# Optimization experiments

Hardware: AMD Instinct MI355X
Metric: run time of the kernel (lower is better)

The kernel has to match this reference:

```python
import jax, jax.numpy as jnp
import numpy as np

B, DIM, H, W = 64, 512, 16, 20
HID = DIM // 2          # 256, MutualAttention hidden
HEADS = 8
NZ, NX = 64, 256        # template (8x8) and search (16x16) token counts
EPS_NORM = 1e-12
EPS_LN = 1e-5


def setup_inputs() -> dict:
    key = jax.random.key(0)
    ks = jax.random.split(key, 16)
    s = 0.02
    return {
        "x1": jax.random.normal(ks[0], (B, DIM, H, W), jnp.float32),
        "x2": jax.random.normal(ks[1], (B, DIM, H, W), jnp.float32),
        "W_lin": jax.random.normal(ks[2], (DIM, 2 * DIM), jnp.float32) * s,
        "b_lin": jnp.zeros((2 * DIM,), jnp.float32),
        "W_down": jax.random.normal(ks[3], (DIM, HID), jnp.float32) * s,
        "b_down": jnp.zeros((HID,), jnp.float32),
        "W_up": jax.random.normal(ks[4], (HID, DIM), jnp.float32) * s,
        "b_up": jnp.zeros((DIM,), jnp.float32),
        "Wq": jax.random.normal(ks[5], (HID, HID), jnp.float32) * s,
        "Wk": jax.random.normal(ks[6], (HID, HID), jnp.float32) * s,
        "Wv": jax.random.normal(ks[7], (HID, HID), jnp.float32) * s,
        "Wo": jax.random.normal(ks[8], (HID, HID), jnp.float32) * s,
        "temperature": jnp.ones((HEADS, 1, 1), jnp.float32),
        "W_end": jax.random.normal(ks[9], (DIM, DIM), jnp.float32) * s,
        "b_end": jnp.zeros((DIM,), jnp.float32),
        "gamma": jnp.ones((DIM,), jnp.float32),
        "beta": jnp.zeros((DIM,), jnp.float32),
    }


def _l2norm(x):
    n = jnp.sqrt(jnp.sum(x * x, axis=-1, keepdims=True))
    return x / jnp.maximum(n, EPS_NORM)


def _branch(zx, zy, W_down, b_down, W_up, b_up, Wq, Wk, Wv, Wo, temperature):
    # zx, zy: [B, n, DIM] tokens; conv1x1 == per-token linear so spatial reshape is a no-op
    res = zx
    a = jax.nn.relu(zx @ W_down + b_down)   # [B, n, HID]  (k, v source)
    b_ = jax.nn.relu(zy @ W_down + b_down)  # [B, n, HID]  (q source)
    xb = jnp.swapaxes(a, 1, 2)              # [B, HID, n]
    yb = jnp.swapaxes(b_, 1, 2)
    res1 = xb
    q = jnp.einsum('oc,bcn->bon', Wq, yb)
    k = jnp.einsum('oc,bcn->bon', Wk, xb)
    v = jnp.einsum('oc,bcn->bon', Wv, xb)
    bsz, _, n = q.shape
    c = HID // HEADS
    q = _l2norm(q.reshape(bsz, HEADS, c, n))
    k = _l2norm(k.reshape(bsz, HEADS, c, n))
    v = v.reshape(bsz, HEADS, c, n)
    attn = jnp.einsum('bhcn,bhdn->bhcd', q, k) * temperature  # [B, H, c, c]
    attn = jax.nn.softmax(attn, axis=-1)
    out = jnp.einsum('bhcd,bhdn->bhcn', attn, v).reshape(bsz, HID, n)
    out = jnp.einsum('oc,bcn->bon', Wo, out)
    out = res1 + out                          # [B, HID, n]
    tok = jnp.swapaxes(out, 1, 2)             # [B, n, HID]
    return res + tok @ W_up + b_up            # [B, n, DIM]


def reference(x1, x2, W_lin, b_lin, W_down, b_down, W_up, b_up,
              Wq, Wk, Wv, Wo, temperature, W_end, b_end, gamma, beta):
    bsz = x1.shape[0]
    t1 = jnp.swapaxes(x1.reshape(bsz, DIM, H * W), 1, 2)  # [B, N, DIM]
    t2 = jnp.swapaxes(x2.reshape(bsz, DIM, H * W), 1, 2)
    h1 = jax.nn.relu(t1 @ W_lin + b_lin)
    h2 = jax.nn.relu(t2 @ W_lin + b_lin)
    y1, u1 = h1[..., :DIM], h1[..., DIM:]
    y2, u2 = h2[..., :DIM], h2[..., DIM:]
    # MutualAttention: template tokens (first 64) and search tokens (rest)
    o_z = _branch(u1[:, :NZ], u2[:, :NZ], W_down, b_down, W_up, b_up, Wq, Wk, Wv, Wo, temperature)
    o_x = _branch(u1[:, NZ:], u2[:, NZ:], W_down, b_down, W_up, b_up, Wq, Wk, Wv, Wo, temperature)
    v1 = jnp.concatenate([o_z, o_x], axis=1)  # [B, N, DIM]
    y = y1 + v1
    pre = t1 + (y @ W_end + b_end)
    mu = jnp.mean(pre, axis=-1, keepdims=True)
    var = jnp.mean((pre - mu) ** 2, axis=-1, keepdims=True)
    ln = (pre - mu) / jnp.sqrt(var + EPS_LN) * gamma + beta
    return jnp.swapaxes(ln, 1, 2).reshape(bsz, DIM, H, W)
```

## Files before the change

kernel.cpp:

```cpp
#include <hip/hip_runtime.h>
#include <math.h>

#define NTOK 320
#define BB   64
#define DIMC 512
#define HIDC 256
#define NHEAD 8

#define F_BIAS 1
#define F_RELU 2
#define F_RES1 4
#define F_RES2 8

#define BM 128
#define BN 64
#define BK 32

typedef __attribute__((ext_vector_type(8))) short bf8_t;
typedef __attribute__((ext_vector_type(4))) float f4_t;

__device__ __forceinline__ void bsplit(float f, short& h, short& l) {
    const unsigned u = __float_as_uint(f);
    h = (short)(u >> 16);
    const float fh = __uint_as_float(u & 0xffff0000u);
    const float fl = f - fh;
    l = (short)(__float_as_uint(fl) >> 16);
}

template<int FLAGS>
__global__ __launch_bounds__(256)
void gemm_mfma(const float* __restrict__ W, int ldw,
               const float* __restrict__ X, long sX,
               float* __restrict__ C, long sC,
               int Dk,
               const float* __restrict__ bias,
               const float* __restrict__ R1, long sR1,
               const float* __restrict__ R2, long sR2)
{
    __shared__ float Ws[BK][BM];
    __shared__ float Xs[BK][BN];

    const int b  = blockIdx.z;
    const int j0 = blockIdx.x * BM;
    const int n0 = blockIdx.y * BN;
    const float* Xb = X + (long)b * sX;

    const int t    = threadIdx.x;
    const int wave = t >> 6;
    const int lane = t & 63;
    const int wm   = wave >> 1;
    const int wn   = wave & 1;
    const int r16  = lane & 15;
    const int g    = lane >> 4;

    f4_t acc[4][2];
    #pragma unroll
    for (int i = 0; i < 4; ++i)
        #pragma unroll
        for (int j = 0; j < 2; ++j)
            acc[i][j] = (f4_t){0.f, 0.f, 0.f, 0.f};

    for (int d0 = 0; d0 < Dk; d0 += BK) {
        #pragma unroll
        for (int i = 0; i < 4; ++i) {
            const int slot = t + (i << 8);
            const int k = slot >> 5;
            const int c = slot & 31;
            const f4_t v = *(const f4_t*)&W[(long)(d0 + k) * ldw + j0 + (c << 2)];
            const int cs = c ^ ((k >> 3) << 2);
            *(f4_t*)&Ws[k][cs << 2] = v;
        }
        #pragma unroll
        for (int i = 0; i < 2; ++i) {
            const int slot = t + (i << 8);
            const int k = slot >> 4;
            const int c = slot & 15;
            const f4_t v = *(const f4_t*)&Xb[(long)(d0 + k) * NTOK + n0 + (c << 2)];
            const int cs = c ^ ((k >> 3) << 2);
            *(f4_t*)&Xs[k][cs << 2] = v;
        }
        __syncthreads();

        bf8_t ah[4], al[4], bh[2], bl[2];
        #pragma unroll
        for (int fm = 0; fm < 4; ++fm) {
            const int m  = wm * 64 + fm * 16 + r16;
            const int col = (((m >> 2) ^ (g << 2)) << 2) | (m & 3);
            #pragma unroll
            for (int e = 0; e < 8; ++e) {
                short h, l;
                bsplit(Ws[g * 8 + e][col], h, l);
                ah[fm][e] = h; al[fm][e] = l;
            }
        }
        #pragma unroll
        for (int fn = 0; fn < 2; ++fn) {
            const int n  = wn * 32 + fn * 16 + r16;
            const int col = (((n >> 2) ^ (g << 2)) << 2) | (n & 3);
            #pragma unroll
            for (int e = 0; e < 8; ++e) {
                short h, l;
                bsplit(Xs[g * 8 + e][col], h, l);
                bh[fn][e] = h; bl[fn][e] = l;
            }
        }

        #pragma unroll
        for (int fm = 0; fm < 4; ++fm)
            #pragma unroll
            for (int fn = 0; fn < 2; ++fn) {
                acc[fm][fn] = __builtin_amdgcn_mfma_f32_16x16x32_bf16(ah[fm], bh[fn], acc[fm][fn], 0, 0, 0);
                acc[fm][fn] = __builtin_amdgcn_mfma_f32_16x16x32_bf16(ah[fm], bl[fn], acc[fm][fn], 0, 0, 0);
                acc[fm][fn] = __builtin_amdgcn_mfma_f32_16x16x32_bf16(al[fm], bh[fn], acc[fm][fn], 0, 0, 0);
            }
        __syncthreads();
    }

    float* Cb = C + (long)b * sC;
    #pragma unroll
    for (int fm = 0; fm < 4; ++fm) {
        #pragma unroll
        for (int reg = 0; reg < 4; ++reg) {
            const int m = j0 + wm * 64 + fm * 16 + g * 4 + reg;
            float bv = 0.f;
            if (FLAGS & F_BIAS) bv = bias[m];
            #pragma unroll
            for (int fn = 0; fn < 2; ++fn) {
                const int n = n0 + wn * 32 + fn * 16 + r16;
                float v = acc[fm][fn][reg] + bv;
                if (FLAGS & F_RES1) v += R1[(long)b * sR1 + (long)m * NTOK + n];
                if (FLAGS & F_RES2) v += R2[(long)b * sR2 + (long)m * NTOK + n];
                if (FLAGS & F_RELU) v = fmaxf(v, 0.f);
                Cb[(long)m * NTOK + n] = v;
            }
        }
    }
}

__global__ __launch_bounds__(256)
void transpose4_k(const float* __restrict__ Wq, const float* __restrict__ Wk,
                  const float* __restrict__ Wv, const float* __restrict__ Wo,
                  float* __restrict__ out)
{
    __shared__ float tile[32][33];
    const float* src = (blockIdx.z == 0) ? Wq : (blockIdx.z == 1) ? Wk
                     : (blockIdx.z == 2) ? Wv : Wo;
    float* dst = out + (long)blockIdx.z * 65536;
    const int x0 = blockIdx.x << 5, y0 = blockIdx.y << 5;
    const int tx = threadIdx.x & 31, ty = threadIdx.x >> 5;
    for (int i = ty; i < 32; i += 8)
        tile[i][tx] = src[(long)(y0 + i) * 256 + x0 + tx];
    __syncthreads();
    for (int i = ty; i < 32; i += 8)
        dst[(long)(x0 + i) * 256 + y0 + tx] = tile[tx][i];
}

__global__ __launch_bounds__(256)
void attn_kernel(const float* __restrict__ Q, const float* __restrict__ K,
                 const float* __restrict__ V, float* __restrict__ O,
                 const float* __restrict__ temp)
{
    const int slice = blockIdx.x;
    const int h     = blockIdx.y;
    const int b     = blockIdx.z;
    const int n0    = slice ? 64 : 0;
    const int Nt    = slice ? 256 : 64;

    __shared__ float qs[32][260], ks[32][260], vs[32][260];
    __shared__ float P[32][36];
    __shared__ float invq[32], invk[32];

    const long base = (long)b * HIDC * NTOK + (long)h * 32 * NTOK + n0;
    const int t = threadIdx.x;
    const int nf4 = Nt >> 2;

    for (int idx = t; idx < 32 * nf4; idx += 256) {
        const int r  = idx / nf4;
        const int n4 = (idx % nf4) << 2;
        *(float4*)&qs[r][n4] = *(const float4*)&Q[base + (long)r * NTOK + n4];
        *(float4*)&ks[r][n4] = *(const float4*)&K[base + (long)r * NTOK + n4];
        *(float4*)&vs[r][n4] = *(const float4*)&V[base + (long)r * NTOK + n4];
    }
    __syncthreads();

    {
        const int r = t >> 3, l8 = t & 7;
        float sq = 0.f, sk = 0.f;
        for (int k4 = l8; k4 < nf4; k4 += 8) {
            const float4 a = *(const float4*)&qs[r][k4 << 2];
            sq = fmaf(a.x,a.x, fmaf(a.y,a.y, fmaf(a.z,a.z, fmaf(a.w,a.w, sq))));
            const float4 c = *(const float4*)&ks[r][k4 << 2];
            sk = fmaf(c.x,c.x, fmaf(c.y,c.y, fmaf(c.z,c.z, fmaf(c.w,c.w, sk))));
        }
        sq += __shfl_xor(sq, 1); sq += __shfl_xor(sq, 2); sq += __shfl_xor(sq, 4);
        sk += __shfl_xor(sk, 1); sk += __shfl_xor(sk, 2); sk += __shfl_xor(sk, 4);
        if (l8 == 0) {
            invq[r] = 1.f / fmaxf(sqrtf(sq), 1e-12f);
            invk[r] = 1.f / fmaxf(sqrtf(sk), 1e-12f);
        }
    }
    __syncthreads();

    {
        const int c = t >> 3, db = (t & 7) << 2;
        float s0 = 0.f, s1 = 0.f, s2 = 0.f, s3 = 0.f;
        for (int n = 0; n < Nt; n += 4) {
            const float4 qv = *(const float4*)&qs[c][n];
            const float4 k0 = *(const float4*)&ks[db + 0][n];
            const float4 k1 = *(const float4*)&ks[db + 1][n];
            const float4 k2 = *(const float4*)&ks[db + 2][n];
            const float4 k3 = *(const float4*)&ks[db + 3][n];
            s0 = fmaf(qv.x,k0.x, fmaf(qv.y,k0.y, fmaf(qv.z,k0.z, fmaf(qv.w,k0.w, s0))));
            s1 = fmaf(qv.x,k1.x, fmaf(qv.y,k1.y, fmaf(qv.z,k1.z, fmaf(qv.w,k1.w, s1))));
            s2 = fmaf(qv.x,k2.x, fmaf(qv.y,k2.y, fmaf(qv.z,k2.z, fmaf(qv.w,k2.w, s2))));
            s3 = fmaf(qv.x,k3.x, fmaf(qv.y,k3.y, fmaf(qv.z,k3.z, fmaf(qv.w,k3.w, s3))));
        }
        const float sc = invq[c] * temp[h];
        float l0 = s0 * sc * invk[db + 0];
        float l1 = s1 * sc * invk[db + 1];
        float l2 = s2 * sc * invk[db + 2];
        float l3 = s3 * sc * invk[db + 3];
        float m = fmaxf(fmaxf(l0, l1), fmaxf(l2, l3));
        m = fmaxf(m, __shfl_xor(m, 1));
        m = fmaxf(m, __shfl_xor(m, 2));
        m = fmaxf(m, __shfl_xor(m, 4));
        const float e0 = expf(l0 - m), e1 = expf(l1 - m);
        const float e2 = expf(l2 - m), e3 = expf(l3 - m);
        float sum = e0 + e1 + e2 + e3;
        sum += __shfl_xor(sum, 1); sum += __shfl_xor(sum, 2); sum += __shfl_xor(sum, 4);
        const float inv = 1.f / sum;
        P[c][db + 0] = e0 * inv; P[c][db + 1] = e1 * inv;
        P[c][db + 2] = e2 * inv; P[c][db + 3] = e3 * inv;
    }
    __syncthreads();

    for (int idx = t; idx < 32 * nf4; idx += 256) {
        const int c  = idx / nf4;
        const int n4 = (idx % nf4) << 2;
        float4 o = make_float4(0.f, 0.f, 0.f, 0.f);
        #pragma unroll
        for (int d = 0; d < 32; ++d) {
            const float p = P[c][d];
            const float4 vv = *(const float4*)&vs[d][n4];
            o.x = fmaf(p, vv.x, o.x); o.y = fmaf(p, vv.y, o.y);
            o.z = fmaf(p, vv.z, o.z); o.w = fmaf(p, vv.w, o.w);
        }
        *(float4*)&O[base + (long)c * NTOK + n4] = o;
    }
}

__global__ __launch_bounds__(256)
void ln_kernel(const float* __restrict__ Pre, const float* __restrict__ gamma,
               const float* __restrict__ beta, float* __restrict__ out)
{
    const int b  = blockIdx.y;
    const int n  = (blockIdx.x << 6) + (threadIdx.x & 63);
    const int q  = threadIdx.x >> 6;
    const float* Pb = Pre + (long)b * DIMC * NTOK;
    float s = 0.f, s2 = 0.f;
    for (int d = q; d < DIMC; d += 4) {
        const float v = Pb[(long)d * NTOK + n];
        s += v; s2 = fmaf(v, v, s2);
    }
    __shared__ float sb[4][64], s2b[4][64];
    sb[q][threadIdx.x & 63] = s;
    s2b[q][threadIdx.x & 63] = s2;
    __syncthreads();
    float ts = 0.f, ts2 = 0.f;
    #pragma unroll
    for (int i = 0; i < 4; ++i) { ts += sb[i][threadIdx.x & 63]; ts2 += s2b[i][threadIdx.x & 63]; }
    const float mu   = ts * (1.f / 512.f);
    const float var  = ts2 * (1.f / 512.f) - mu * mu;
    const float rstd = 1.f / sqrtf(var + 1e-5f);
    float* Ob = out + (long)b * DIMC * NTOK;
    for (int d = q; d < DIMC; d += 4) {
        const float v = Pb[(long)d * NTOK + n];
        Ob[(long)d * NTOK + n] = (v - mu) * rstd * gamma[d] + beta[d];
    }
}

extern "C" void kernel_launch(void* const* d_in, const int* in_sizes, int n_in,
                              void* d_out, int out_size, void* d_ws, size_t ws_size,
                              hipStream_t stream)
{
    const float* x1     = (const float*)d_in[0];
    const float* x2     = (const float*)d_in[1];
    const float* W_lin  = (const float*)d_in[2];
    const float* b_lin  = (const float*)d_in[3];
    const float* W_down = (const float*)d_in[4];
    const float* b_down = (const float*)d_in[5];
    const float* W_up   = (const float*)d_in[6];
    const float* b_up   = (const float*)d_in[7];
    const float* Wq     = (const float*)d_in[8];
    const float* Wk     = (const float*)d_in[9];
    const float* Wv     = (const float*)d_in[10];
    const float* Wo     = (const float*)d_in[11];
    const float* temp   = (const float*)d_in[12];
    const float* W_end  = (const float*)d_in[13];
    const float* b_end  = (const float*)d_in[14];
    const float* gamma  = (const float*)d_in[15];
    const float* beta   = (const float*)d_in[16];

    float* ws = (float*)d_ws;
    const long s512  = (long)DIMC * NTOK;
    const long s1024 = 2L * s512;
    const long s256  = (long)HIDC * NTOK;

    float* H1  = ws;
    float* U2  = H1 + (long)BB * 1024 * NTOK;
    float* XB  = U2 + (long)BB * 512 * NTOK;
    float* YB  = XB + (long)BB * 256 * NTOK;
    float* Qb  = YB + (long)BB * 256 * NTOK;
    float* Kb  = Qb + (long)BB * 256 * NTOK;
    float* Vb  = Kb + (long)BB * 256 * NTOK;
    float* WT  = Vb + (long)BB * 256 * NTOK;
    float* Y1   = H1;
    float* U1   = H1 + 512 * NTOK;
    float* AO   = YB;
    float* OUTC = Qb;
    float* PRE  = U2;

    const dim3 blk(256);

    transpose4_k<<<dim3(8, 8, 4), blk, 0, stream>>>(Wq, Wk, Wv, Wo, WT);

    gemm_mfma<F_BIAS | F_RELU><<<dim3(8, 5, BB), blk, 0, stream>>>(
        W_lin, 1024, x1, s512, H1, s1024, 512, b_lin, nullptr, 0, nullptr, 0);
    gemm_mfma<F_BIAS | F_RELU><<<dim3(4, 5, BB), blk, 0, stream>>>(
        W_lin + 512, 1024, x2, s512, U2, s512, 512, b_lin + 512, nullptr, 0, nullptr, 0);
    gemm_mfma<F_BIAS | F_RELU><<<dim3(2, 5, BB), blk, 0, stream>>>(
        W_down, 256, U1, s1024, XB, s256, 512, b_down, nullptr, 0, nullptr, 0);
    gemm_mfma<F_BIAS | F_RELU><<<dim3(2, 5, BB), blk, 0, stream>>>(
        W_down, 256, U2, s512, YB, s256, 512, b_down, nullptr, 0, nullptr, 0);
    gemm_mfma<0><<<dim3(2, 5, BB), blk, 0, stream>>>(
        WT + 0 * 65536, 256, YB, s256, Qb, s256, 256, nullptr, nullptr, 0, nullptr, 0);
    gemm_mfma<0><<<dim3(2, 5, BB), blk, 0, stream>>>(
        WT + 1 * 65536, 256, XB, s256, Kb, s256, 256, nullptr, nullptr, 0, nullptr, 0);
    gemm_mfma<0><<<dim3(2, 5, BB), blk, 0, stream>>>(
        WT + 2 * 65536, 256, XB, s256, Vb, s256, 256, nullptr, nullptr, 0, nullptr, 0);
    attn_kernel<<<dim3(2, NHEAD, BB), blk, 0, stream>>>(Qb, Kb, Vb, AO, temp);
    gemm_mfma<F_RES1><<<dim3(2, 5, BB), blk, 0, stream>>>(
        WT + 3 * 65536, 256, AO, s256, OUTC, s256, 256, nullptr, XB, s256, nullptr, 0);
    gemm_mfma<F_BIAS | F_RES1 | F_RES2><<<dim3(4, 5, BB), blk, 0, stream>>>(
        W_up, 512, OUTC, s256, Y1, s1024, 256, b_up, U1, s1024, Y1, s1024);
    gemm_mfma<F_BIAS | F_RES1><<<dim3(4, 5, BB), blk, 0, stream>>>(
        W_end, 512, Y1, s1024, PRE, s512, 512, b_end, x1, s512, nullptr, 0);
    ln_kernel<<<dim3(5, BB), blk, 0, stream>>>(PRE, gamma, beta, (float*)d_out);
}
```

Before: 648.7 us.

## Switch pipeline to token-major layout with pre-split bf16 hi/lo operands

Reworks the whole pipeline to a token-major row layout. Inputs and weights are pre-split once into bf16 high/low halves, so the GEMM inner loop loads ready MFMA fragments from LDS instead of splitting floats on every tile. Intermediates are stored as packed bf16 pairs, K and V are fused into one GEMM, and the attention and layernorm kernels are rewritten for the new layout. This adds extra packing kernels and transposes and doubles the number of intermediate buffers written, in exchange for less per-tile conversion work and contiguous fragment loads.

```diff
diff --git a/kernel.cpp b/kernel.cpp
--- a/kernel.cpp
+++ b/kernel.cpp
@@ -3,55 +3,105 @@
 
 #define NTOK 320
 #define BB   64
+#define RTOT (BB * NTOK)
 #define DIMC 512
 #define HIDC 256
 #define NHEAD 8
 
-#define F_BIAS 1
-#define F_RELU 2
-#define F_RES1 4
-#define F_RES2 8
-
-#define BM 128
-#define BN 64
-#define BK 32
-
+typedef unsigned short u16;
 typedef __attribute__((ext_vector_type(8))) short bf8_t;
 typedef __attribute__((ext_vector_type(4))) float f4_t;
-
-__device__ __forceinline__ void bsplit(float f, short& h, short& l) {
+typedef __attribute__((ext_vector_type(4))) unsigned short us4_t;
+typedef __attribute__((ext_vector_type(4))) unsigned int  u4_t;
+
+#define F_BIAS  1
+#define F_RELU  2
+#define F_F32   4
+#define F_PACK  8
+#define F_RES1P 16
+#define F_RES2P 32
+#define F_RESX1 64
+
+__device__ __forceinline__ void bsplit(float f, u16& h, u16& l) {
     const unsigned u = __float_as_uint(f);
-    h = (short)(u >> 16);
-    const float fh = __uint_as_float(u & 0xffff0000u);
-    const float fl = f - fh;
-    l = (short)(__float_as_uint(fl) >> 16);
+    h = (u16)(u >> 16);
+    const float fl = f - __uint_as_float(u & 0xffff0000u);
+    l = (u16)(__float_as_uint(fl) >> 16);
+}
+__device__ __forceinline__ float brecon(u16 h, u16 l) {
+    return __uint_as_float((unsigned)h << 16) + __uint_as_float((unsigned)l << 16);
+}
+
+__global__ __launch_bounds__(256)
+void pack_w_k(const float* __restrict__ Wlin, const float* __restrict__ Wdown,
+              const float* __restrict__ Wup,  const float* __restrict__ Wend,
+              const float* __restrict__ Wq,   const float* __restrict__ Wk,
+              const float* __restrict__ Wv,   const float* __restrict__ Wo,
+              u16* __restrict__ Ph, u16* __restrict__ Pl)
+{
+    const int idx = blockIdx.x * 256 + threadIdx.x;
+    if (idx >= 1310720) return;
+    float v;
+    int i = idx;
+    if      (i < 524288) { const int j = i >> 9, d = i & 511; v = Wlin[d * 1024 + j]; }
+    else if (i < 655360) { i -= 524288; const int j = i >> 9, d = i & 511; v = Wdown[d * 256 + j]; }
+    else if (i < 786432) { i -= 655360; const int j = i >> 8, d = i & 255; v = Wup[d * 512 + j]; }
+    else if (i < 1048576){ i -= 786432; const int j = i >> 9, d = i & 511; v = Wend[d * 512 + j]; }
+    else if (i < 1114112){ v = Wq[i - 1048576]; }
+    else if (i < 1245184){ i -= 1114112; v = (i < 65536) ? Wk[i] : Wv[i - 65536]; }
+    else                 { v = Wo[i - 1245184]; }
+    u16 h, l; bsplit(v, h, l);
+    Ph[idx] = h; Pl[idx] = l;
+}
+
+__global__ __launch_bounds__(256)
+void pack_x_k(const float* __restrict__ x1, const float* __restrict__ x2,
+              u16* __restrict__ X1h, u16* __restrict__ X1l,
+              u16* __restrict__ X2h, u16* __restrict__ X2l)
+{
+    __shared__ float tile[64 * 65];
+    const int b = blockIdx.z & 63, which = blockIdx.z >> 6;
+    const float* src = which ? x2 : x1;
+    u16* Dh = which ? X2h : X1h;
+    u16* Dl = which ? X2l : X1l;
+    const int c0 = blockIdx.x << 6, n0 = blockIdx.y << 6;
+    const int t = threadIdx.x, col = t & 63, rq = t >> 6;
+    const float* sb_ = src + (long)b * DIMC * NTOK;
+    #pragma unroll
+    for (int i = 0; i < 16; ++i) {
+        const int c = rq * 16 + i;
+        tile[c * 65 + col] = sb_[(long)(c0 + c) * NTOK + n0 + col];
+    }
+    __syncthreads();
+    #pragma unroll
+    for (int i = 0; i < 16; ++i) {
+        const int nr = rq * 16 + i;
+        u16 h, l; bsplit(tile[col * 65 + nr], h, l);
+        const long o = (long)(b * NTOK + n0 + nr) * DIMC + c0 + col;
+        Dh[o] = h; Dl[o] = l;
+    }
 }
 
 template<int FLAGS>
 __global__ __launch_bounds__(256)
-void gemm_mfma(const float* __restrict__ W, int ldw,
-               const float* __restrict__ X, long sX,
-               float* __restrict__ C, long sC,
-               int Dk,
-               const float* __restrict__ bias,
-               const float* __restrict__ R1, long sR1,
-               const float* __restrict__ R2, long sR2)
-{
-    __shared__ float Ws[BK][BM];
-    __shared__ float Xs[BK][BN];
-
-    const int b  = blockIdx.z;
-    const int j0 = blockIdx.x * BM;
-    const int n0 = blockIdx.y * BN;
-    const float* Xb = X + (long)b * sX;
-
-    const int t    = threadIdx.x;
-    const int wave = t >> 6;
-    const int lane = t & 63;
-    const int wm   = wave >> 1;
-    const int wn   = wave & 1;
-    const int r16  = lane & 15;
-    const int g    = lane >> 4;
+void gemm_tm(const u16* __restrict__ Agh, const u16* __restrict__ Agl,
+             const u16* __restrict__ Bgh, const u16* __restrict__ Bgl,
+             int Dk,
+             float* __restrict__ Cf, int ldcf,
+             u16* __restrict__ Ch, u16* __restrict__ Cl, int ldcp,
+             const float* __restrict__ bias,
+             const u16* __restrict__ R1h, const u16* __restrict__ R1l, int ldr1,
+             const u16* __restrict__ R2h, const u16* __restrict__ R2l, int ldr2,
+             const float* __restrict__ xres)
+{
+    __shared__ __align__(16) u16 Ah[128 * 40], Al[128 * 40];
+    __shared__ __align__(16) u16 Bh[64 * 40],  Bl[64 * 40];
+
+    const int j0 = blockIdx.x * 128;
+    const int r0 = blockIdx.y * 64;
+    const int t = threadIdx.x, lane = t & 63, wave = t >> 6;
+    const int wm = wave >> 1, wn = wave & 1;
+    const int r16 = lane & 15, g = lane >> 4;
 
     f4_t acc[4][2];
     #pragma unroll
@@ -60,51 +110,35 @@
         for (int j = 0; j < 2; ++j)
             acc[i][j] = (f4_t){0.f, 0.f, 0.f, 0.f};
 
-    for (int d0 = 0; d0 < Dk; d0 += BK) {
-        #pragma unroll
-        for (int i = 0; i < 4; ++i) {
-            const int slot = t + (i << 8);
-            const int k = slot >> 5;
-            const int c = slot & 31;
-            const f4_t v = *(const f4_t*)&W[(long)(d0 + k) * ldw + j0 + (c << 2)];
-            const int cs = c ^ ((k >> 3) << 2);
-            *(f4_t*)&Ws[k][cs << 2] = v;
-        }
-        #pragma unroll
-        for (int i = 0; i < 2; ++i) {
-            const int slot = t + (i << 8);
-            const int k = slot >> 4;
-            const int c = slot & 15;
-            const f4_t v = *(const f4_t*)&Xb[(long)(d0 + k) * NTOK + n0 + (c << 2)];
-            const int cs = c ^ ((k >> 3) << 2);
-            *(f4_t*)&Xs[k][cs << 2] = v;
+    for (int d0 = 0; d0 < Dk; d0 += 32) {
+        {
+            const int row0 = t >> 2,        c0_ = (t & 3) << 3;
+            const int row1 = (t >> 2) + 64;
+            const long a0 = (long)(j0 + row0) * Dk + d0 + c0_;
+            const long a1 = (long)(j0 + row1) * Dk + d0 + c0_;
+            *(u4_t*)&Ah[row0 * 40 + c0_] = *(const u4_t*)&Agh[a0];
+            *(u4_t*)&Ah[row1 * 40 + c0_] = *(const u4_t*)&Agh[a1];
+            *(u4_t*)&Al[row0 * 40 + c0_] = *(const u4_t*)&Agl[a0];
+            *(u4_t*)&Al[row1 * 40 + c0_] = *(const u4_t*)&Agl[a1];
+            const long ab = (long)(r0 + row0) * Dk + d0 + c0_;
+            *(u4_t*)&Bh[row0 * 40 + c0_] = *(const u4_t*)&Bgh[ab];
+            *(u4_t*)&Bl[row0 * 40 + c0_] = *(const u4_t*)&Bgl[ab];
         }
         __syncthreads();
 
         bf8_t ah[4], al[4], bh[2], bl[2];
         #pragma unroll
         for (int fm = 0; fm < 4; ++fm) {
-            const int m  = wm * 64 + fm * 16 + r16;
-            const int col = (((m >> 2) ^ (g << 2)) << 2) | (m & 3);
-            #pragma unroll
-            for (int e = 0; e < 8; ++e) {
-                short h, l;
-                bsplit(Ws[g * 8 + e][col], h, l);
-                ah[fm][e] = h; al[fm][e] = l;
-            }
+            const int m = wm * 64 + fm * 16 + r16;
+            ah[fm] = *(const bf8_t*)&Ah[m * 40 + g * 8];
+            al[fm] = *(const bf8_t*)&Al[m * 40 + g * 8];
         }
         #pragma unroll
         for (int fn = 0; fn < 2; ++fn) {
-            const int n  = wn * 32 + fn * 16 + r16;
-            const int col = (((n >> 2) ^ (g << 2)) << 2) | (n & 3);
-            #pragma unroll
-            for (int e = 0; e < 8; ++e) {
-                short h, l;
-                bsplit(Xs[g * 8 + e][col], h, l);
-                bh[fn][e] = h; bl[fn][e] = l;
-            }
-        }
-
+            const int rr = wn * 32 + fn * 16 + r16;
+            bh[fn] = *(const bf8_t*)&Bh[rr * 40 + g * 8];
+            bl[fn] = *(const bf8_t*)&Bl[rr * 40 + g * 8];
+        }
         #pragma unroll
         for (int fm = 0; fm < 4; ++fm)
             #pragma unroll
@@ -116,87 +150,88 @@
         __syncthreads();
     }
 
-    float* Cb = C + (long)b * sC;
+    const int bb = r0 / NTOK, nn0 = r0 % NTOK;
     #pragma unroll
     for (int fm = 0; fm < 4; ++fm) {
-        #pragma unroll
-        for (int reg = 0; reg < 4; ++reg) {
-            const int m = j0 + wm * 64 + fm * 16 + g * 4 + reg;
-            float bv = 0.f;
-            if (FLAGS & F_BIAS) bv = bias[m];
-            #pragma unroll
-            for (int fn = 0; fn < 2; ++fn) {
-                const int n = n0 + wn * 32 + fn * 16 + r16;
-                float v = acc[fm][fn][reg] + bv;
-                if (FLAGS & F_RES1) v += R1[(long)b * sR1 + (long)m * NTOK + n];
-                if (FLAGS & F_RES2) v += R2[(long)b * sR2 + (long)m * NTOK + n];
-                if (FLAGS & F_RELU) v = fmaxf(v, 0.f);
-                Cb[(long)m * NTOK + n] = v;
+        const int jb = j0 + wm * 64 + fm * 16 + g * 4;
+        f4_t bv = (f4_t){0.f, 0.f, 0.f, 0.f};
+        if (FLAGS & F_BIAS) bv = *(const f4_t*)&bias[jb];
+        #pragma unroll
+        for (int fn = 0; fn < 2; ++fn) {
+            const int r = r0 + wn * 32 + fn * 16 + r16;
+            f4_t v = acc[fm][fn];
+            if (FLAGS & F_BIAS) v += bv;
+            if (FLAGS & F_RES1P) {
+                const us4_t rh = *(const us4_t*)&R1h[(long)r * ldr1 + jb];
+                const us4_t rl = *(const us4_t*)&R1l[(long)r * ldr1 + jb];
+                #pragma unroll
+                for (int q = 0; q < 4; ++q) v[q] += brecon(rh[q], rl[q]);
+            }
+            if (FLAGS & F_RES2P) {
+                const us4_t rh = *(const us4_t*)&R2h[(long)r * ldr2 + jb];
+                const us4_t rl = *(const us4_t*)&R2l[(long)r * ldr2 + jb];
+                #pragma unroll
+                for (int q = 0; q < 4; ++q) v[q] += brecon(rh[q], rl[q]);
+            }
+            if (FLAGS & F_RESX1) {
+                const int nl = nn0 + wn * 32 + fn * 16 + r16;
+                #pragma unroll
+                for (int q = 0; q < 4; ++q)
+                    v[q] += xres[(long)bb * DIMC * NTOK + (long)(jb + q) * NTOK + nl];
+            }
+            if (FLAGS & F_RELU) {
+                #pragma unroll
+                for (int q = 0; q < 4; ++q) v[q] = fmaxf(v[q], 0.f);
+            }
+            if (FLAGS & F_F32)
+                *(f4_t*)&Cf[(long)r * ldcf + jb] = v;
+            if (FLAGS & F_PACK) {
+                us4_t h4, l4;
+                #pragma unroll
+                for (int q = 0; q < 4; ++q) { u16 h, l; bsplit(v[q], h, l); h4[q] = h; l4[q] = l; }
+                *(us4_t*)&Ch[(long)r * ldcp + jb] = h4;
+                *(us4_t*)&Cl[(long)r * ldcp + jb] = l4;
             }
         }
     }
 }
 
 __global__ __launch_bounds__(256)
-void transpose4_k(const float* __restrict__ Wq, const float* __restrict__ Wk,
-                  const float* __restrict__ Wv, const float* __restrict__ Wo,
-                  float* __restrict__ out)
-{
-    __shared__ float tile[32][33];
-    const float* src = (blockIdx.z == 0) ? Wq : (blockIdx.z == 1) ? Wk
-                     : (blockIdx.z == 2) ? Wv : Wo;
-    float* dst = out + (long)blockIdx.z * 65536;
-    const int x0 = blockIdx.x << 5, y0 = blockIdx.y << 5;
-    const int tx = threadIdx.x & 31, ty = threadIdx.x >> 5;
-    for (int i = ty; i < 32; i += 8)
-        tile[i][tx] = src[(long)(y0 + i) * 256 + x0 + tx];
-    __syncthreads();
-    for (int i = ty; i < 32; i += 8)
-        dst[(long)(x0 + i) * 256 + y0 + tx] = tile[tx][i];
-}
-
-__global__ __launch_bounds__(256)
-void attn_kernel(const float* __restrict__ Q, const float* __restrict__ K,
-                 const float* __restrict__ V, float* __restrict__ O,
-                 const float* __restrict__ temp)
-{
-    const int slice = blockIdx.x;
-    const int h     = blockIdx.y;
-    const int b     = blockIdx.z;
-    const int n0    = slice ? 64 : 0;
-    const int Nt    = slice ? 256 : 64;
-
-    __shared__ float qs[32][260], ks[32][260], vs[32][260];
-    __shared__ float P[32][36];
+void attn_tm(const float* __restrict__ Qf, const float* __restrict__ KVf,
+             u16* __restrict__ AOh, u16* __restrict__ AOl,
+             const float* __restrict__ temp)
+{
+    const int slice = blockIdx.x, h = blockIdx.y, b = blockIdx.z;
+    const int rb = b * NTOK + (slice ? 64 : 0);
+    const int Nt = slice ? 256 : 64;
+    const int qc = h * 32;
+
+    __shared__ float ks[256 * 33], vs[256 * 33];
+    __shared__ float PT[32 * 36];
     __shared__ float invq[32], invk[32];
-
-    const long base = (long)b * HIDC * NTOK + (long)h * 32 * NTOK + n0;
     const int t = threadIdx.x;
-    const int nf4 = Nt >> 2;
-
-    for (int idx = t; idx < 32 * nf4; idx += 256) {
-        const int r  = idx / nf4;
-        const int n4 = (idx % nf4) << 2;
-        *(float4*)&qs[r][n4] = *(const float4*)&Q[base + (long)r * NTOK + n4];
-        *(float4*)&ks[r][n4] = *(const float4*)&K[base + (long)r * NTOK + n4];
-        *(float4*)&vs[r][n4] = *(const float4*)&V[base + (long)r * NTOK + n4];
+
+    for (int q = t; q < Nt * 8; q += 256) {
+        const int n = q >> 3, c4 = (q & 7) << 2;
+        *(f4_t*)&ks[n * 33 + c4] = *(const f4_t*)&KVf[(long)(rb + n) * 512 + qc + c4];
+        *(f4_t*)&vs[n * 33 + c4] = *(const f4_t*)&KVf[(long)(rb + n) * 512 + 256 + qc + c4];
     }
     __syncthreads();
 
     {
-        const int r = t >> 3, l8 = t & 7;
+        const int c = t >> 3, l8 = t & 7;
         float sq = 0.f, sk = 0.f;
-        for (int k4 = l8; k4 < nf4; k4 += 8) {
-            const float4 a = *(const float4*)&qs[r][k4 << 2];
-            sq = fmaf(a.x,a.x, fmaf(a.y,a.y, fmaf(a.z,a.z, fmaf(a.w,a.w, sq))));
-            const float4 c = *(const float4*)&ks[r][k4 << 2];
-            sk = fmaf(c.x,c.x, fmaf(c.y,c.y, fmaf(c.z,c.z, fmaf(c.w,c.w, sk))));
+        for (int n = l8; n < Nt; n += 8) {
+            const float qv = Qf[(long)(rb + n) * 256 + qc + c];
+            sq = fmaf(qv, qv, sq);
+            const float kv = ks[n * 33 + c];
+            sk = fmaf(kv, kv, sk);
         }
         sq += __shfl_xor(sq, 1); sq += __shfl_xor(sq, 2); sq += __shfl_xor(sq, 4);
         sk += __shfl_xor(sk, 1); sk += __shfl_xor(sk, 2); sk += __shfl_xor(sk, 4);
         if (l8 == 0) {
-            invq[r] = 1.f / fmaxf(sqrtf(sq), 1e-12f);
-            invk[r] = 1.f / fmaxf(sqrtf(sk), 1e-12f);
+            invq[c] = 1.f / fmaxf(sqrtf(sq), 1e-12f);
+            invk[c] = 1.f / fmaxf(sqrtf(sk), 1e-12f);
         }
     }
     __syncthreads();
@@ -205,77 +240,104 @@
         const int c = t >> 3, db = (t & 7) << 2;
         float s0 = 0.f, s1 = 0.f, s2 = 0.f, s3 = 0.f;
         for (int n = 0; n < Nt; n += 4) {
-            const float4 qv = *(const float4*)&qs[c][n];
-            const float4 k0 = *(const float4*)&ks[db + 0][n];
-            const float4 k1 = *(const float4*)&ks[db + 1][n];
-            const float4 k2 = *(const float4*)&ks[db + 2][n];
-            const float4 k3 = *(const float4*)&ks[db + 3][n];
-            s0 = fmaf(qv.x,k0.x, fmaf(qv.y,k0.y, fmaf(qv.z,k0.z, fmaf(qv.w,k0.w, s0))));
-            s1 = fmaf(qv.x,k1.x, fmaf(qv.y,k1.y, fmaf(qv.z,k1.z, fmaf(qv.w,k1.w, s1))));
-            s2 = fmaf(qv.x,k2.x, fmaf(qv.y,k2.y, fmaf(qv.z,k2.z, fmaf(qv.w,k2.w, s2))));
-            s3 = fmaf(qv.x,k3.x, fmaf(qv.y,k3.y, fmaf(qv.z,k3.z, fmaf(qv.w,k3.w, s3))));
+            #pragma unroll
+            for (int u = 0; u < 4; ++u) {
+                const float qv = Qf[(long)(rb + n + u) * 256 + qc + c];
+                const int o = (n + u) * 33 + db;
+                s0 = fmaf(qv, ks[o + 0], s0);
+                s1 = fmaf(qv, ks[o + 1], s1);
+                s2 = fmaf(qv, ks[o + 2], s2);
+                s3 = fmaf(qv, ks[o + 3], s3);
+            }
         }
         const float sc = invq[c] * temp[h];
-        float l0 = s0 * sc * invk[db + 0];
-        float l1 = s1 * sc * invk[db + 1];
-        float l2 = s2 * sc * invk[db + 2];
-        float l3 = s3 * sc * invk[db + 3];
+        const float l0 = s0 * sc * invk[db + 0];
+        const float l1 = s1 * sc * invk[db + 1];
+        const float l2 = s2 * sc * invk[db + 2];
+        const float l3 = s3 * sc * invk[db + 3];
         float m = fmaxf(fmaxf(l0, l1), fmaxf(l2, l3));
         m = fmaxf(m, __shfl_xor(m, 1));
         m = fmaxf(m, __shfl_xor(m, 2));
         m = fmaxf(m, __shfl_xor(m, 4));
         const float e0 = expf(l0 - m), e1 = expf(l1 - m);
         const float e2 = expf(l2 - m), e3 = expf(l3 - m);
-        float sum = e0 + e1 + e2 + e3;
-        sum += __shfl_xor(sum, 1); sum += __shfl_xor(sum, 2); sum += __shfl_xor(sum, 4);
-        const float inv = 1.f / sum;
-        P[c][db + 0] = e0 * inv; P[c][db + 1] = e1 * inv;
-        P[c][db + 2] = e2 * inv; P[c][db + 3] = e3 * inv;
-    }
-    __syncthreads();
-
-    for (int idx = t; idx < 32 * nf4; idx += 256) {
-        const int c  = idx / nf4;
-        const int n4 = (idx % nf4) << 2;
-        float4 o = make_float4(0.f, 0.f, 0.f, 0.f);
-        #pragma unroll
+        float s = e0 + e1 + e2 + e3;
+        s += __shfl_xor(s, 1); s += __shfl_xor(s, 2); s += __shfl_xor(s, 4);
+        const float inv = 1.f / s;
+        PT[(db + 0) * 36 + c] = e0 * inv;
+        PT[(db + 1) * 36 + c] = e1 * inv;
+        PT[(db + 2) * 36 + c] = e2 * inv;
+        PT[(db + 3) * 36 + c] = e3 * inv;
+    }
+    __syncthreads();
+
+    for (int idx = t; idx < Nt * 8; idx += 256) {
+        const int n = idx >> 3, cq = (idx & 7) << 2;
+        f4_t o = (f4_t){0.f, 0.f, 0.f, 0.f};
+        #pragma unroll 8
         for (int d = 0; d < 32; ++d) {
-            const float p = P[c][d];
-            const float4 vv = *(const float4*)&vs[d][n4];
-            o.x = fmaf(p, vv.x, o.x); o.y = fmaf(p, vv.y, o.y);
-            o.z = fmaf(p, vv.z, o.z); o.w = fmaf(p, vv.w, o.w);
-        }
-        *(float4*)&O[base + (long)c * NTOK + n4] = o;
+            const float vv = vs[n * 33 + d];
+            const f4_t p = *(const f4_t*)&PT[d * 36 + cq];
+            o += p * vv;
+        }
+        us4_t h4, l4;
+        #pragma unroll
+        for (int q = 0; q < 4; ++q) { u16 h, l; bsplit(o[q], h, l); h4[q] = h; l4[q] = l; }
+        const long oadr = (long)(rb + n) * 256 + qc + cq;
+        *(us4_t*)&AOh[oadr] = h4;
+        *(us4_t*)&AOl[oadr] = l4;
     }
 }
 
 __global__ __launch_bounds__(256)
-void ln_kernel(const float* __restrict__ Pre, const float* __restrict__ gamma,
-               const float* __restrict__ beta, float* __restrict__ out)
-{
-    const int b  = blockIdx.y;
-    const int n  = (blockIdx.x << 6) + (threadIdx.x & 63);
-    const int q  = threadIdx.x >> 6;
-    const float* Pb = Pre + (long)b * DIMC * NTOK;
-    float s = 0.f, s2 = 0.f;
-    for (int d = q; d < DIMC; d += 4) {
-        const float v = Pb[(long)d * NTOK + n];
-        s += v; s2 = fmaf(v, v, s2);
-    }
-    __shared__ float sb[4][64], s2b[4][64];
-    sb[q][threadIdx.x & 63] = s;
-    s2b[q][threadIdx.x & 63] = s2;
-    __syncthreads();
-    float ts = 0.f, ts2 = 0.f;
-    #pragma unroll
-    for (int i = 0; i < 4; ++i) { ts += sb[i][threadIdx.x & 63]; ts2 += s2b[i][threadIdx.x & 63]; }
-    const float mu   = ts * (1.f / 512.f);
-    const float var  = ts2 * (1.f / 512.f) - mu * mu;
-    const float rstd = 1.f / sqrtf(var + 1e-5f);
-    float* Ob = out + (long)b * DIMC * NTOK;
-    for (int d = q; d < DIMC; d += 4) {
-        const float v = Pb[(long)d * NTOK + n];
-        Ob[(long)d * NTOK + n] = (v - mu) * rstd * gamma[d] + beta[d];
+void ln_tm(const float* __restrict__ PREf, const float* __restrict__ gamma,
+           const float* __restrict__ beta, float* __restrict__ out)
+{
+    __shared__ float tile[64 * 65];
+    __shared__ float sb[64 * 4], s2b[64 * 4];
+    __shared__ float muS[64], rsS[64];
+    const int r0 = blockIdx.x << 6;
+    const int b = r0 / NTOK, n0 = r0 % NTOK;
+    const int t = threadIdx.x;
+    {
+        const int tok = t >> 2, qq = t & 3;
+        const float* row = PREf + (long)(r0 + tok) * 512 + qq * 128;
+        float s = 0.f, s2 = 0.f;
+        #pragma unroll 8
+        for (int i = 0; i < 32; ++i) {
+            const f4_t v4 = *(const f4_t*)&row[i * 4];
+            s += v4[0] + v4[1] + v4[2] + v4[3];
+            s2 = fmaf(v4[0], v4[0], s2); s2 = fmaf(v4[1], v4[1], s2);
+            s2 = fmaf(v4[2], v4[2], s2); s2 = fmaf(v4[3], v4[3], s2);
+        }
+        sb[tok * 4 + qq] = s; s2b[tok * 4 + qq] = s2;
+    }
+    __syncthreads();
+    if (t < 64) {
+        const float s  = sb[t * 4] + sb[t * 4 + 1] + sb[t * 4 + 2] + sb[t * 4 + 3];
+        const float s2 = s2b[t * 4] + s2b[t * 4 + 1] + s2b[t * 4 + 2] + s2b[t * 4 + 3];
+        const float mu = s * (1.f / 512.f);
+        const float var = s2 * (1.f / 512.f) - mu * mu;
+        muS[t] = mu;
+        rsS[t] = 1.f / sqrtf(var + 1e-5f);
+    }
+    __syncthreads();
+    const int cc = t & 63, tq = t >> 6;
+    for (int ct = 0; ct < 8; ++ct) {
+        const float ga = gamma[ct * 64 + cc], be = beta[ct * 64 + cc];
+        #pragma unroll
+        for (int i = 0; i < 16; ++i) {
+            const int tok = tq * 16 + i;
+            const float v = PREf[(long)(r0 + tok) * 512 + ct * 64 + cc];
+            tile[cc * 65 + tok] = (v - muS[tok]) * rsS[tok] * ga + be;
+        }
+        __syncthreads();
+        #pragma unroll
+        for (int i = 0; i < 16; ++i) {
+            const int ccr = tq * 16 + i;
+            out[(long)b * DIMC * NTOK + (long)(ct * 64 + ccr) * NTOK + n0 + cc] = tile[ccr * 65 + cc];
+        }
+        __syncthreads();
     }
 }
 
@@ -301,49 +363,82 @@
     const float* gamma  = (const float*)d_in[15];
     const float* beta   = (const float*)d_in[16];
 
-    float* ws = (float*)d_ws;
-    const long s512  = (long)DIMC * NTOK;
-    const long s1024 = 2L * s512;
-    const long s256  = (long)HIDC * NTOK;
-
-    float* H1  = ws;
-    float* U2  = H1 + (long)BB * 1024 * NTOK;
-    float* XB  = U2 + (long)BB * 512 * NTOK;
-    float* YB  = XB + (long)BB * 256 * NTOK;
-    float* Qb  = YB + (long)BB * 256 * NTOK;
-    float* Kb  = Qb + (long)BB * 256 * NTOK;
-    float* Vb  = Kb + (long)BB * 256 * NTOK;
-    float* WT  = Vb + (long)BB * 256 * NTOK;
-    float* Y1   = H1;
-    float* U1   = H1 + 512 * NTOK;
-    float* AO   = YB;
-    float* OUTC = Qb;
-    float* PRE  = U2;
+    const size_t MB = 1ull << 20;
+    char* base = (char*)d_ws;
+    u16* X1h = (u16*)(base + 0 * MB);
+    u16* X1l = (u16*)(base + 20 * MB);
+    u16* X2h = (u16*)(base + 40 * MB);
+    u16* X2l = (u16*)(base + 60 * MB);
+    u16* Wph = (u16*)(base + 80 * MB);
+    u16* Wpl = (u16*)(base + 80 * MB + 2621440);
+    u16* Y1h = (u16*)(base + 85 * MB);
+    u16* Y1l = (u16*)(base + 105 * MB);
+    u16* U1h = (u16*)(base + 125 * MB);
+    u16* U1l = (u16*)(base + 145 * MB);
+    u16* U2h = (u16*)(base + 165 * MB);
+    u16* U2l = (u16*)(base + 185 * MB);
+    u16* XBh = (u16*)(base + 205 * MB);
+    u16* XBl = (u16*)(base + 215 * MB);
+    float* Qf  = (float*)(base + 0 * MB);
+    u16* AOh   = (u16*)(base + 20 * MB);
+    u16* AOl   = (u16*)(base + 30 * MB);
+    u16* OCh   = (u16*)(base + 0 * MB);
+    u16* OCl   = (u16*)(base + 10 * MB);
+    u16* YBh   = (u16*)(base + 40 * MB);
+    u16* YBl   = (u16*)(base + 50 * MB);
+    float* KVf = (float*)(base + 40 * MB);
+    float* PREf= (float*)(base + 40 * MB);
+    u16* Yh    = (u16*)(base + 165 * MB);
+    u16* Yl    = (u16*)(base + 185 * MB);
+
+    const long WL = 0, WD = 524288, WU = 655360, WE = 786432,
+               WQ = 1048576, WKV = 1114112, WO = 1245184;
 
     const dim3 blk(256);
 
-    transpose4_k<<<dim3(8, 8, 4), blk, 0, stream>>>(Wq, Wk, Wv, Wo, WT);
-
-    gemm_mfma<F_BIAS | F_RELU><<<dim3(8, 5, BB), blk, 0, stream>>>(
-        W_lin, 1024, x1, s512, H1, s1024, 512, b_lin, nullptr, 0, nullptr, 0);
-    gemm_mfma<F_BIAS | F_RELU><<<dim3(4, 5, BB), blk, 0, stream>>>(
-        W_lin + 512, 1024, x2, s512, U2, s512, 512, b_lin + 512, nullptr, 0, nullptr, 0);
-    gemm_mfma<F_BIAS | F_RELU><<<dim3(2, 5, BB), blk, 0, stream>>>(
-        W_down, 256, U1, s1024, XB, s256, 512, b_down, nullptr, 0, nullptr, 0);
-    gemm_mfma<F_BIAS | F_RELU><<<dim3(2, 5, BB), blk, 0, stream>>>(
-        W_down, 256, U2, s512, YB, s256, 512, b_down, nullptr, 0, nullptr, 0);
-    gemm_mfma<0><<<dim3(2, 5, BB), blk, 0, stream>>>(
-        WT + 0 * 65536, 256, YB, s256, Qb, s256, 256, nullptr, nullptr, 0, nullptr, 0);
-    gemm_mfma<0><<<dim3(2, 5, BB), blk, 0, stream>>>(
-        WT + 1 * 65536, 256, XB, s256, Kb, s256, 256, nullptr, nullptr, 0, nullptr, 0);
-    gemm_mfma<0><<<dim3(2, 5, BB), blk, 0, stream>>>(
-        WT + 2 * 65536, 256, XB, s256, Vb, s256, 256, nullptr, nullptr, 0, nullptr, 0);
-    attn_kernel<<<dim3(2, NHEAD, BB), blk, 0, stream>>>(Qb, Kb, Vb, AO, temp);
-    gemm_mfma<F_RES1><<<dim3(2, 5, BB), blk, 0, stream>>>(
-        WT + 3 * 65536, 256, AO, s256, OUTC, s256, 256, nullptr, XB, s256, nullptr, 0);
-    gemm_mfma<F_BIAS | F_RES1 | F_RES2><<<dim3(4, 5, BB), blk, 0, stream>>>(
-        W_up, 512, OUTC, s256, Y1, s1024, 256, b_up, U1, s1024, Y1, s1024);
-    gemm_mfma<F_BIAS | F_RES1><<<dim3(4, 5, BB), blk, 0, stream>>>(
-        W_end, 512, Y1, s1024, PRE, s512, 512, b_end, x1, s512, nullptr, 0);
-    ln_kernel<<<dim3(5, BB), blk, 0, stream>>>(PRE, gamma, beta, (float*)d_out);
-}
+    pack_x_k<<<dim3(8, 5, 128), blk, 0, stream>>>(x1, x2, X1h, X1l, X2h, X2l);
+    pack_w_k<<<dim3(5120), blk, 0, stream>>>(W_lin, W_down, W_up, W_end, Wq, Wk, Wv, Wo, Wph, Wpl);
+
+    gemm_tm<F_BIAS | F_RELU | F_PACK><<<dim3(4, 320), blk, 0, stream>>>(
+        Wph + WL, Wpl + WL, X1h, X1l, 512,
+        nullptr, 0, Y1h, Y1l, 512, b_lin,
+        nullptr, nullptr, 0, nullptr, nullptr, 0, nullptr);
+    gemm_tm<F_BIAS | F_RELU | F_PACK><<<dim3(4, 320), blk, 0, stream>>>(
+        Wph + WL + 512 * 512, Wpl + WL + 512 * 512, X1h, X1l, 512,
+        nullptr, 0, U1h, U1l, 512, b_lin + 512,
+        nullptr, nullptr, 0, nullptr, nullptr, 0, nullptr);
+    gemm_tm<F_BIAS | F_RELU | F_PACK><<<dim3(4, 320), blk, 0, stream>>>(
+        Wph + WL + 512 * 512, Wpl + WL + 512 * 512, X2h, X2l, 512,
+        nullptr, 0, U2h, U2l, 512, b_lin + 512,
+        nullptr, nullptr, 0, nullptr, nullptr, 0, nullptr);
+    gemm_tm<F_BIAS | F_RELU | F_PACK><<<dim3(2, 320), blk, 0, stream>>>(
+        Wph + WD, Wpl + WD, U1h, U1l, 512,
+        nullptr, 0, XBh, XBl, 256, b_down,
+        nullptr, nullptr, 0, nullptr, nullptr, 0, nullptr);
+    gemm_tm<F_BIAS | F_RELU | F_PACK><<<dim3(2, 320), blk, 0, stream>>>(
+        Wph + WD, Wpl + WD, U2h, U2l, 512,
+        nullptr, 0, YBh, YBl, 256, b_down,
+        nullptr, nullptr, 0, nullptr, nullptr, 0, nullptr);
+    gemm_tm<F_F32><<<dim3(2, 320), blk, 0, stream>>>(
+        Wph + WQ, Wpl + WQ, YBh, YBl, 256,
+        Qf, 256, nullptr, nullptr, 0, nullptr,
+        nullptr, nullptr, 0, nullptr, nullptr, 0, nullptr);
+    gemm_tm<F_F32><<<dim3(4, 320), blk, 0, stream>>>(
+        Wph + WKV, Wpl + WKV, XBh, XBl, 256,
+        KVf, 512, nullptr, nullptr, 0, nullptr,
+        nullptr, nullptr, 0, nullptr, nullptr, 0, nullptr);
+    attn_tm<<<dim3(2, NHEAD, BB), blk, 0, stream>>>(Qf, KVf, AOh, AOl, temp);
+    gemm_tm<F_PACK | F_RES1P><<<dim3(2, 320), blk, 0, stream>>>(
+        Wph + WO, Wpl + WO, AOh, AOl, 256,
+        nullptr, 0, OCh, OCl, 256, nullptr,
+        XBh, XBl, 256, nullptr, nullptr, 0, nullptr);
+    gemm_tm<F_BIAS | F_PACK | F_RES1P | F_RES2P><<<dim3(4, 320), blk, 0, stream>>>(
+        Wph + WU, Wpl + WU, OCh, OCl, 256,
+        nullptr, 0, Yh, Yl, 512, b_up,
+        Y1h, Y1l, 512, U1h, U1l, 512, nullptr);
+    gemm_tm<F_BIAS | F_F32 | F_RESX1><<<dim3(4, 320), blk, 0, stream>>>(
+        Wph + WE, Wpl + WE, Yh, Yl, 512,
+        PREf, 512, nullptr, nullptr, 0, b_end,
+        nullptr, nullptr, 0, nullptr, nullptr, 0, x1);
+    ln_tm<<<dim3(320), blk, 0, stream>>>(PREf, gamma, beta, (float*)d_out);
+}
```

Result: slower. 669.1 us (+3.1%).
